# Kernel tuning notes

Hardware: AMD Instinct MI355X
Metric: run time of the kernel (lower is better)

The kernel has to match this reference:

```python
import jax, jax.numpy as jnp
import numpy as np
from jax import lax

T, B = 32, 16
NUM_ACTIONS = 18
HID = 256
C_V, C_K, C_S, NQ = 120, 8, 64, 4
NKEY, NVAL = C_K + C_S, C_V + C_S
Hh, Ww = 27, 20


def _spatial_basis():
    # Fourier spatial basis from Mott et al.; U = V = 8 -> 64 channels.
    h, w, U = Hh, Ww, 8
    p_h = np.arange(1, h + 1)[:, None] * np.ones((1, w)) * (np.pi / h)
    p_w = np.ones((h, 1)) * np.arange(1, w + 1)[None, :] * (np.pi / w)
    u = np.arange(1, U + 1)
    a = np.cos(p_h[:, :, None] * u)  # (h,w,8)
    b = np.cos(p_w[:, :, None] * u)  # (h,w,8)
    S = np.einsum('hwu,hwv->hwuv', a, b).reshape(h, w, U * U)
    return jnp.asarray(S, jnp.float32)

_S = _spatial_basis()


def _conv(x, w, b, stride, pad):
    y = lax.conv_general_dilated(x, w, stride, pad,
                                 dimension_numbers=('NCHW', 'OIHW', 'NCHW'))
    return y + b[None, :, None, None]


def setup_inputs() -> dict:
    key = jax.random.key(0)
    ks = iter(jax.random.split(key, 40))
    f32 = jnp.float32
    def rn(shape, s=0.05):
        return jax.random.normal(next(ks), shape, dtype=f32) * s
    return dict(
        frame=jax.random.normal(next(ks), (T, B, 3, 210, 160), dtype=f32),
        done=jnp.zeros((T, B), dtype=bool),
        last_action=jax.random.randint(next(ks), (T, B), 0, NUM_ACTIONS),
        reward=jax.random.normal(next(ks), (T, B), dtype=f32),
        core_h=jnp.zeros((B, HID), f32), core_c=jnp.zeros((B, HID), f32),
        conv_h=jnp.zeros((B, HID // 2, Hh, Ww), f32),
        conv_c=jnp.zeros((B, HID // 2, Hh, Ww), f32),
        cnn_w1=rn((32, 3, 8, 8)), cnn_b1=rn((32,)),
        cnn_w2=rn((64, 32, 4, 4)), cnn_b2=rn((64,)),
        lstm_w=rn((512, 192, 3, 3)), lstm_b=rn((512,)),
        qw1=rn((HID, 128)), qb1=rn((128,)),
        qw2=rn((128, NQ * NKEY)), qb2=rn((NQ * NKEY,)),
        qw3=rn((NQ * NKEY, NQ * NKEY)), qb3=rn((NQ * NKEY,)),
        aw1=rn((NVAL * NQ + NKEY * NQ + 1 + NUM_ACTIONS, 2 * HID)), ab1=rn((2 * HID,)),
        aw2=rn((2 * HID, HID)), ab2=rn((HID,)),
        w_ih=rn((4 * HID, HID)), w_hh=rn((4 * HID, HID)),
        b_ih=rn((4 * HID,)), b_hh=rn((4 * HID,)),
        pw=rn((HID, NUM_ACTIONS)), pb=rn((NUM_ACTIONS,)),
        vw=rn((HID, 1)), vb=rn((1,)),
    )


def reference(frame, done, last_action, reward, core_h, core_c, conv_h, conv_c,
              cnn_w1, cnn_b1, cnn_w2, cnn_b2, lstm_w, lstm_b,
              qw1, qb1, qw2, qb2, qw3, qb3, aw1, ab1, aw2, ab2,
              w_ih, w_hh, b_ih, b_hh, pw, pb, vw, vb):
    x = frame.reshape(T * B, 3, 210, 160)
    x = _conv(x, cnn_w1, cnn_b1, (4, 4), [(1, 1), (2, 2)])
    x = _conv(x, cnn_w2, cnn_b2, (2, 2), [(2, 2), (1, 1)])  # (T*B,64,27,20)
    x = x.reshape(T, B, 64, Hh, Ww)
    nd = (~done).astype(jnp.float32)  # (T,B)

    def vis_step(carry, inp):
        h, c = carry
        x_t, nd_t = inp
        m = nd_t[:, None, None, None]
        h, c = m * h, m * c
        gates = _conv(jnp.concatenate([x_t, h], axis=1), lstm_w, lstm_b,
                      (1, 1), [(1, 1), (1, 1)])
        ai, af, ao, ag = jnp.split(gates, 4, axis=1)
        c = jax.nn.sigmoid(af) * c + jax.nn.sigmoid(ai) * jnp.tanh(ag)
        h = jax.nn.sigmoid(ao) * jnp.tanh(c)
        return (h, c), h

    (vh, vc), O = lax.scan(vis_step, (conv_h, conv_c), (x, nd))
    # Faithful to the original `.view(N, h, w, c)` (a reinterpret, not a transpose).
    O = O.reshape(T * B, Hh, Ww, 128)
    Sb = jnp.broadcast_to(_S, (T * B, Hh, Ww, C_S))
    K = jnp.concatenate([O[..., :C_K], Sb], axis=3).reshape(T, B, Hh, Ww, NKEY)
    V = jnp.concatenate([O[..., C_K:], Sb], axis=3).reshape(T, B, Hh, Ww, NVAL)

    a1h = jax.nn.one_hot(last_action, NUM_ACTIONS, dtype=jnp.float32)  # (T,B,A)
    r = jnp.clip(reward, -1.0, 1.0)[..., None]  # (T,B,1)

    def core_step(carry, inp):
        h, c = carry
        K_t, V_t, r_t, a_t, nd_t = inp
        q = jax.nn.relu(h @ qw1 + qb1)
        q = jax.nn.relu(q @ qw2 + qb2)
        q = (q @ qw3 + qb3).reshape(B, NQ, NKEY)
        A = jnp.einsum('bhwk,bqk->bhwq', K_t, q)
        A = jax.nn.softmax(A.reshape(B, Hh * Ww, NQ), axis=1).reshape(B, Hh, Ww, NQ)
        ans = jnp.einsum('bhwq,bhwv->bqv', A, V_t)  # (B,NQ,NVAL)
        answer = jnp.concatenate(
            [ans.reshape(B, -1), q.reshape(B, -1), r_t, a_t], axis=1)
        ci = jax.nn.relu(answer @ aw1 + ab1) @ aw2 + ab2
        m = nd_t[:, None]
        h, c = m * h, m * c
        gates = ci @ w_ih.T + b_ih + h @ w_hh.T + b_hh  # torch gate order i,f,g,o
        gi, gf, gg, go = jnp.split(gates, 4, axis=1)
        c = jax.nn.sigmoid(gf) * c + jax.nn.sigmoid(gi) * jnp.tanh(gg)
        h = jax.nn.sigmoid(go) * jnp.tanh(c)
        return (h, c), h

    (ch, cc), outs = lax.scan(core_step, (core_h, core_c), (K, V, r, a1h, nd))
    out = outs.reshape(T * B, HID)
    logits = out @ pw + pb
    values = out @ vw + vb
    action = jnp.argmax(logits, axis=1)  # eval-mode action selection
    return (logits.reshape(T, B, NUM_ACTIONS), values.reshape(T, B),
            action.reshape(T, B), ch, cc, vh, vc)
```

## Files before the change

kernel.cpp:

```cpp
#include <hip/hip_runtime.h>
#include <math.h>

#define T_ 32
#define B_ 16
#define NA 18
#define P_ 540

typedef __attribute__((ext_vector_type(8)))  short short8;
typedef __attribute__((ext_vector_type(16))) float f32x16;

__device__ __forceinline__ float sigm(float x){ return 1.0f/(1.0f+expf(-x)); }
__device__ __forceinline__ unsigned short f2bf(float f){
    unsigned u = __float_as_uint(f);
    u += 0x7fff + ((u>>16)&1u);
    return (unsigned short)(u>>16);
}
__device__ __forceinline__ float bfu(unsigned short u){ return __uint_as_float(((unsigned)u)<<16); }

__global__ __launch_bounds__(256) void conv1k(const float* __restrict__ frame,
                                              const float* __restrict__ w,
                                              const float* __restrict__ bias,
                                              unsigned short* __restrict__ c1pad){
    __shared__ float tile[4032];
    int bid = blockIdx.x;
    int n = bid / 52, oh = bid % 52;
    int tid = threadIdx.x;
    const float* fb = frame + (size_t)n*3*210*160;
    for (int s = tid; s < 4032; s += 256){
        int col = s % 168;
        int row = (s/168) & 7;
        int ic  = s / 1344;
        int iy = oh*4 - 1 + row;
        int ix = col - 2;
        float v = 0.f;
        if (iy >= 0 && iy < 210 && ix >= 0 && ix < 160) v = fb[ic*33600 + iy*160 + ix];
        tile[s] = v;
    }
    __syncthreads();
    int oc = tid & 31, grp = tid >> 5;
    float acc[5] = {0.f,0.f,0.f,0.f,0.f};
    const float* wb = w + oc*192;
    for (int ic=0; ic<3; ++ic){
        #pragma unroll
        for (int kh=0; kh<8; ++kh){
            const float* wr = wb + ic*64 + kh*8;
            float4 w0 = *((const float4*)wr);
            float4 w1 = *((const float4*)(wr+4));
            const float* row = tile + ic*1344 + kh*168 + grp*20;
            float r[24];
            *((float4*)(r+ 0)) = *((const float4*)(row+ 0));
            *((float4*)(r+ 4)) = *((const float4*)(row+ 4));
            *((float4*)(r+ 8)) = *((const float4*)(row+ 8));
            *((float4*)(r+12)) = *((const float4*)(row+12));
            *((float4*)(r+16)) = *((const float4*)(row+16));
            *((float4*)(r+20)) = *((const float4*)(row+20));
            #pragma unroll
            for (int o=0;o<5;++o){
                acc[o] += r[o*4+0]*w0.x + r[o*4+1]*w0.y + r[o*4+2]*w0.z + r[o*4+3]*w0.w
                        + r[o*4+4]*w1.x + r[o*4+5]*w1.y + r[o*4+6]*w1.z + r[o*4+7]*w1.w;
            }
        }
    }
    float bi = bias[oc];
    unsigned short* ob = c1pad + ((size_t)(n*32 + oc)*56 + oh+2)*42 + 1;
    #pragma unroll
    for (int o=0;o<5;++o) ob[grp*5+o] = f2bf(acc[o] + bi);
}

__global__ void apack2k(const float* __restrict__ w2, unsigned short* __restrict__ ap){
    int idx = blockIdx.x*256 + threadIdx.x;
    if (idx >= 32768) return;
    int j = idx & 7;
    int lane = (idx>>3) & 63;
    int mt = (idx>>9) & 1;
    int ic = idx >> 10;
    int k = ((lane>>5)<<3) + j;
    int oc = mt*32 + (lane & 31);
    ap[idx] = f2bf(w2[((oc*32 + ic)<<4) + k]);
}

__global__ __launch_bounds__(256) void c2mfma(const unsigned short* __restrict__ c1pad,
                                              const unsigned short* __restrict__ apack2,
                                              const float* __restrict__ bias,
                                              unsigned short* __restrict__ xpad){
    __shared__ unsigned short p2[2][3072];
    __shared__ float bsm[64];
    int bid = blockIdx.x;
    int s = bid / 5;
    int n0 = (bid % 5) * 128;
    int tid = threadIdx.x;
    int wave = tid >> 6, lane = tid & 63;
    int khalf = (lane>>5) << 3;
    if (tid < 64) bsm[tid] = bias[tid];
    const unsigned short* cb = c1pad + (size_t)s*32*2352;

    int soff[8], swaddr[8];
    #pragma unroll
    for (int q=0;q<8;++q){
        int idx = q*256 + tid;
        int n = idx & 127, k = idx >> 7;
        int p = n0 + n; if (p > 539) p = 539;
        soff[q] = ((p/20)*2 + (k>>2))*42 + (p%20)*2 + (k&3);
        swaddr[q] = n*24 + k;
    }
    #pragma unroll
    for (int q=0;q<8;++q) p2[0][swaddr[q]] = cb[soff[q]];
    unsigned short rv[8];
    #pragma unroll
    for (int q=0;q<8;++q) rv[q] = cb[2352 + soff[q]];

    int mt = wave >> 1, ntb = (wave & 1) * 2;
    short8 acur = *((const short8*)(apack2 + ((size_t)mt*64 + lane)*8));
    short8 anxt;
    f32x16 acc[2];
    #pragma unroll
    for (int jj=0;jj<2;++jj)
        #pragma unroll
        for (int rg=0;rg<16;++rg) acc[jj][rg] = 0.f;
    __syncthreads();

    for (int c=0; c<32; ++c){
        int buf = c & 1;
        if (c < 31){
            #pragma unroll
            for (int q=0;q<8;++q) p2[buf^1][swaddr[q]] = rv[q];
        }
        if (c < 30){
            const unsigned short* src = cb + (size_t)(c+2)*2352;
            #pragma unroll
            for (int q=0;q<8;++q) rv[q] = src[soff[q]];
        }
        if (c < 31) anxt = *((const short8*)(apack2 + ((size_t)((c+1)*2 + mt)*64 + lane)*8));
        #pragma unroll
        for (int jj=0;jj<2;++jj){
            int n = (ntb+jj)*32 + (lane & 31);
            short8 bf = *((const short8*)(&p2[buf][n*24 + khalf]));
            acc[jj] = __builtin_amdgcn_mfma_f32_32x32x16_bf16(acur, bf, acc[jj], 0, 0, 0);
        }
        acur = anxt;
        __syncthreads();
    }
    #pragma unroll
    for (int jj=0;jj<2;++jj){
        int pos = n0 + (ntb+jj)*32 + (lane & 31);
        if (pos >= 540) continue;
        int y = pos/20, x = pos%20;
        unsigned short* op = xpad + (size_t)s*64*640 + (y+1)*22 + x + 1;
        #pragma unroll
        for (int rg=0; rg<16; ++rg){
            int oc = mt*32 + (rg & 3) + 8*(rg>>2) + 4*(lane>>5);
            op[(size_t)oc*640] = f2bf(acc[jj][rg] + bsm[oc]);
        }
    }
}

__global__ void sbasisk(float* __restrict__ S){
    int idx = blockIdx.x*256 + threadIdx.x;
    if (idx >= P_*64) return;
    int s = idx & 63, p = idx >> 6;
    int y = p/20, x = p%20;
    int u = s >> 3, v = s & 7;
    double a  = cos((double)((y+1)*(u+1)) * M_PI / 27.0);
    double bb = cos((double)((x+1)*(v+1)) * M_PI / 20.0);
    S[idx] = (float)(a*bb);
}

__global__ void packw4k(const float* __restrict__ in, unsigned short* __restrict__ out, int R, int C){
    int idx = blockIdx.x*256 + threadIdx.x;
    int r4cnt = (R+3)>>2;
    if (idx >= r4cnt*C*4) return;
    int j = idx & 3;
    int rc = idx >> 2;
    int c = rc % C;
    int r = (rc / C)*4 + j;
    out[idx] = (r < R) ? f2bf(in[(size_t)r*C + c]) : (unsigned short)0;
}
__global__ void packt4k(const float* __restrict__ in, unsigned short* __restrict__ out, int R, int C){
    int idx = blockIdx.x*256 + threadIdx.x;
    int r4cnt = (R+3)>>2;
    if (idx >= r4cnt*C*4) return;
    int j = idx & 3;
    int rc = idx >> 2;
    int c = rc % C;
    int r = (rc / C)*4 + j;
    out[idx] = (r < R) ? f2bf(in[(size_t)c*R + r]) : (unsigned short)0;
}

__global__ void apackk(const float* __restrict__ lw, unsigned short* __restrict__ ap){
    int idx = blockIdx.x*256 + threadIdx.x;
    if (idx >= 1572864) return;
    int j = idx & 7;
    int lane = (idx>>3) & 63;
    int mt = (idx>>9) & 15;
    int ch = idx >> 13;
    int kk = ((lane>>5)<<3) + j;
    int oc = mt*32 + (lane & 31);
    ap[idx] = (kk < 9) ? f2bf(lw[(size_t)oc*1728 + ch*9 + kk]) : (unsigned short)0;
}

__global__ void h0packk(const float* __restrict__ h0, unsigned short* __restrict__ hpad){
    int idx = blockIdx.x*256 + threadIdx.x;
    if (idx >= 16*128*540) return;
    int plane = idx / 540, p = idx % 540;
    hpad[(size_t)plane*640 + (p/20+1)*22 + (p%20) + 1] = f2bf(h0[idx]);
}

__global__ __launch_bounds__(512) void gvck(const unsigned short* __restrict__ xpad,
                                            const unsigned short* __restrict__ hrd,
                                            unsigned short* __restrict__ hwr,
                                            const unsigned short* __restrict__ apack,
                                            const float* __restrict__ lb,
                                            const unsigned char* __restrict__ done,
                                            float* __restrict__ vh, float* __restrict__ vc,
                                            unsigned short* __restrict__ hreA,
                                            const float* __restrict__ S,
                                            const unsigned short* __restrict__ pq1, const float* __restrict__ qb1,
                                            const unsigned short* __restrict__ pq2, const float* __restrict__ qb2,
                                            const unsigned short* __restrict__ pq3, const float* __restrict__ qb3,
                                            const unsigned short* __restrict__ pa1, const float* __restrict__ ab1,
                                            const unsigned short* __restrict__ pa2, const float* __restrict__ ab2,
                                            const unsigned short* __restrict__ pih, const unsigned short* __restrict__ phh,
                                            const float* __restrict__ bih, const float* __restrict__ bhh,
                                            const float* __restrict__ reward, const int* __restrict__ lact,
                                            float* __restrict__ hsb, float* __restrict__ csb,
                                            float* __restrict__ outs,
                                            int t){
    __shared__ __align__(16) unsigned char smraw[65536];
    int bid = blockIdx.x;
    int tid = threadIdx.x;

    if (bid < 288){
        if (t >= T_) return;
        unsigned short (*panel)[6144] = (unsigned short (*)[6144])smraw;
        float* gsm = (float*)smraw;
        int b  = bid % 16;
        int r  = bid / 16;
        int nb = r % 9;
        int mh = r / 9;
        int wave = tid >> 6, lane = tid & 63;
        int khalf = (lane>>5) << 3;
        int n0 = nb * 64;
        bool dn = done[t*B_ + b];

        const unsigned short* xb = xpad + ((size_t)(t*B_ + b))*64*640;
        const unsigned short* hb = hrd + (size_t)b*128*640;

        int soff[5], swaddr[5], gq[5];
        bool act[5];
        #pragma unroll
        for (int q=0;q<5;++q){
            int idx = q*512 + tid;
            act[q] = idx < 2304;
            int idc = act[q] ? idx : 0;
            int g = idc / 576;
            int rr = idc % 576;
            int k = rr / 64, n = rr & 63;
            int p = n0 + n; if (p > 539) p = 539;
            int pbase = (p/20)*22 + (p%20);
            soff[q] = pbase + (k/3)*22 + (k%3);
            swaddr[q] = g*1536 + n*24 + k;
            gq[q] = g;
        }
        for (int s2 = tid; s2 < 3584; s2 += 512){
            int bf2 = s2 / 1792, r2 = s2 % 1792;
            int g2 = r2 / 448, rr2 = r2 % 448;
            panel[bf2][g2*1536 + (rr2 & 63)*24 + 9 + (rr2>>6)] = 0;
        }
        #pragma unroll
        for (int q=0;q<5;++q) if (act[q]) panel[0][swaddr[q]] = xb[gq[q]*640 + soff[q]];
        unsigned short rv[5];
        #pragma unroll
        for (int q=0;q<5;++q) rv[q] = act[q] ? xb[(4+gq[q])*640 + soff[q]] : (unsigned short)0;

        int mt = (wave>>1)*4 + mh*2 + (wave&1);
        short8 acur[4], anxt[4];
        #pragma unroll
        for (int kc=0;kc<4;++kc)
            acur[kc] = *((const short8*)(apack + ((size_t)(kc*16 + mt)*64 + lane)*8));

        f32x16 acc[2];
        #pragma unroll
        for (int j=0;j<2;++j)
            #pragma unroll
            for (int rg=0;rg<16;++rg) acc[j][rg] = 0.f;
        __syncthreads();

        for (int it=0; it<48; ++it){
            int buf = it & 1;
            if (it < 47){
                #pragma unroll
                for (int q=0;q<5;++q) if (act[q]) panel[buf^1][swaddr[q]] = rv[q];
            }
            if (it < 46){
                int icb = (it+2)*4;
                #pragma unroll
                for (int q=0;q<5;++q){
                    if (act[q]){
                        int ic = icb + gq[q];
                        rv[q] = (ic < 64) ? xb[ic*640 + soff[q]]
                                          : (dn ? (unsigned short)0 : hb[(ic-64)*640 + soff[q]]);
                    }
                }
            }
            if (it < 47){
                int cb2 = (it+1)*4;
                #pragma unroll
                for (int kc=0;kc<4;++kc)
                    anxt[kc] = *((const short8*)(apack + ((size_t)((cb2+kc)*16 + mt)*64 + lane)*8));
            }
            #pragma unroll
            for (int kc=0;kc<4;++kc){
                #pragma unroll
                for (int j=0;j<2;++j){
                    int n = j*32 + (lane & 31);
                    short8 bf = *((const short8*)(&panel[buf][kc*1536 + n*24 + khalf]));
                    acc[j] = __builtin_amdgcn_mfma_f32_32x32x16_bf16(acur[kc], bf, acc[j], 0, 0, 0);
                }
            }
            #pragma unroll
            for (int kc=0;kc<4;++kc) acur[kc] = anxt[kc];
            __syncthreads();
        }

        int g8 = wave >> 1, ih = wave & 1;
        #pragma unroll
        for (int j=0;j<2;++j){
            int p_loc = j*32 + (lane & 31);
            #pragma unroll
            for (int rg=0; rg<16; ++rg){
                int c_loc = ih*32 + 4*(lane>>5) + (rg & 3) + 8*(rg>>2);
                gsm[g8*4096 + c_loc*64 + p_loc] = acc[j][rg];
            }
        }
        __syncthreads();

        {
            int p_loc = tid & 63, c0 = tid >> 6;
            int pg = n0 + p_loc;
            if (pg < 540){
                float m = dn ? 0.f : 1.f;
                int y = pg/20, x = pg%20;
                #pragma unroll
                for (int e=0;e<8;++e){
                    int c_loc = c0*8 + e;
                    int cg = mh*64 + c_loc;
                    float gi = gsm[        c_loc*64 + p_loc] + lb[      cg];
                    float gf = gsm[ 4096 + c_loc*64 + p_loc] + lb[128 + cg];
                    float go = gsm[ 8192 + c_loc*64 + p_loc] + lb[256 + cg];
                    float gg = gsm[12288 + c_loc*64 + p_loc] + lb[384 + cg];
                    size_t idx = ((size_t)b*128 + cg)*540 + pg;
                    float cold = vc[idx] * m;
                    float cn = sigm(gf)*cold + sigm(gi)*tanhf(gg);
                    float hn = sigm(go)*tanhf(cn);
                    vc[idx] = cn;
                    if (t == T_-1) vh[idx] = hn;
                    hwr[((size_t)b*128 + cg)*640 + (y+1)*22 + x + 1] = f2bf(hn);
                    int flat = cg*540 + pg;
                    int pos = (flat/2560)*20 + (flat/128)%20;
                    int ch  = flat & 127;
                    hreA[((size_t)(t*B_ + b)*540 + pos)*128 + ch] = f2bf(hn);
                }
            }
        }
        return;
    }

    if (t == 0) return;
    int tc = t - 1;
    int b = bid - 288;
    float* fs = (float*)smraw;
    float* hs   = fs;
    float* cs   = fs + 256;
    float* hs2  = fs + 512;
    float* q1   = fs + 768;
    float* q2   = fs + 896;
    float* q3   = fs + 1184;
    float* elog = fs + 1472;
    float* red  = fs + 3632;
    float* ansv = fs + 3664;
    float* hid  = fs + 4720;
    float* cis  = fs + 5232;
    float* gb   = fs + 5488;

    if (tid < 256){ hs[tid] = hsb[b*256+tid]; cs[tid] = csb[b*256+tid]; }
    if (tid >= 256 && tid < 269) ansv[1043 + (tid-256)] = 0.f;
    __syncthreads();

    float m = done[tc*B_+b] ? 0.f : 1.f;
    if (tid < 128){
        float a0=0.f,a1=0.f,a2=0.f,a3=0.f;
        for (int i4=0;i4<64;++i4){
            ushort4 w = *((const ushort4*)(pq1 + (size_t)((i4<<7)+tid)*4));
            float4 h4 = *((const float4*)(hs + i4*4));
            a0 += h4.x*bfu(w.x); a1 += h4.y*bfu(w.y);
            a2 += h4.z*bfu(w.z); a3 += h4.w*bfu(w.w);
        }
        q1[tid] = fmaxf(qb1[tid] + ((a0+a1)+(a2+a3)), 0.f);
    }
    __syncthreads();
    if (tid < 288){
        float a0=0.f,a1=0.f,a2=0.f,a3=0.f;
        for (int i4=0;i4<32;++i4){
            ushort4 w = *((const ushort4*)(pq2 + (size_t)(i4*288+tid)*4));
            float4 h4 = *((const float4*)(q1 + i4*4));
            a0 += h4.x*bfu(w.x); a1 += h4.y*bfu(w.y);
            a2 += h4.z*bfu(w.z); a3 += h4.w*bfu(w.w);
        }
        q2[tid] = fmaxf(qb2[tid] + ((a0+a1)+(a2+a3)), 0.f);
    }
    __syncthreads();
    if (tid < 288){
        float a0=0.f,a1=0.f,a2=0.f,a3=0.f;
        for (int i4=0;i4<72;++i4){
            ushort4 w = *((const ushort4*)(pq3 + (size_t)(i4*288+tid)*4));
            float4 h4 = *((const float4*)(q2 + i4*4));
            a0 += h4.x*bfu(w.x); a1 += h4.y*bfu(w.y);
            a2 += h4.z*bfu(w.z); a3 += h4.w*bfu(w.w);
        }
        float a = qb3[tid] + ((a0+a1)+(a2+a3));
        q3[tid] = a;
        ansv[736+tid] = a;
    }
    if (tid == 0){ float r = reward[tc*B_+b]; ansv[1024] = fminf(1.f,fmaxf(-1.f,r)); }
    if (tid >= 32 && tid < 32+NA) ansv[1025 + tid-32] = (lact[tc*B_+b] == tid-32) ? 1.f : 0.f;
    __syncthreads();

    const unsigned short* hrb = hreA + (size_t)(tc*B_ + b)*540*128;
    for (int idx = tid; idx < 4*P_; idx += 512){
        int qi = idx / P_, p = idx % P_;
        const unsigned short* hp = hrb + (size_t)p*128;
        uint4 hv = *((const uint4*)hp);
        const float* qv = q3 + qi*72;
        float a = __uint_as_float(hv.x<<16)*qv[0] + __uint_as_float(hv.x & 0xffff0000u)*qv[1]
                + __uint_as_float(hv.y<<16)*qv[2] + __uint_as_float(hv.y & 0xffff0000u)*qv[3]
                + __uint_as_float(hv.z<<16)*qv[4] + __uint_as_float(hv.z & 0xffff0000u)*qv[5]
                + __uint_as_float(hv.w<<16)*qv[6] + __uint_as_float(hv.w & 0xffff0000u)*qv[7];
        const float* Sp = S + p*64;
        #pragma unroll
        for (int s2=0;s2<16;++s2){
            float4 sv = *((const float4*)(Sp + 4*s2));
            a += sv.x*qv[8+4*s2] + sv.y*qv[9+4*s2] + sv.z*qv[10+4*s2] + sv.w*qv[11+4*s2];
        }
        elog[qi*P_ + p] = a;
    }
    __syncthreads();
    {
        int qi = tid >> 7, lt = tid & 127;
        float mx = -1e30f;
        for (int p = lt; p < P_; p += 128) mx = fmaxf(mx, elog[qi*P_ + p]);
        for (int off=32; off; off>>=1) mx = fmaxf(mx, __shfl_down(mx, off));
        if ((tid & 63) == 0) red[tid>>6] = mx;
        __syncthreads();
        if (tid < 4) red[16+tid] = fmaxf(red[2*tid], red[2*tid+1]);
        __syncthreads();
        mx = red[16+qi];
        float sm = 0.f;
        for (int p = lt; p < P_; p += 128){ float e = expf(elog[qi*P_ + p]-mx); elog[qi*P_ + p] = e; sm += e; }
        for (int off=32; off; off>>=1) sm += __shfl_down(sm, off);
        if ((tid & 63) == 0) red[8 + (tid>>6)] = sm;
        __syncthreads();
        if (tid < 4) red[24+tid] = red[8+2*tid] + red[8+2*tid+1];
        __syncthreads();
    }
    if (tid < 240){
        int g = tid >> 2;
        int qi = g / 15, vb = g % 15;
        int pc = tid & 3;
        float ac[8] = {0,0,0,0,0,0,0,0};
        const unsigned short* hb8 = hrb + 8 + vb*8;
        for (int p = pc*135; p < pc*135+135; ++p){
            float e = elog[qi*P_ + p];
            uint4 hv = *((const uint4*)(hb8 + (size_t)p*128));
            ac[0] += e*__uint_as_float(hv.x<<16);
            ac[1] += e*__uint_as_float(hv.x & 0xffff0000u);
            ac[2] += e*__uint_as_float(hv.y<<16);
            ac[3] += e*__uint_as_float(hv.y & 0xffff0000u);
            ac[4] += e*__uint_as_float(hv.z<<16);
            ac[5] += e*__uint_as_float(hv.z & 0xffff0000u);
            ac[6] += e*__uint_as_float(hv.w<<16);
            ac[7] += e*__uint_as_float(hv.w & 0xffff0000u);
        }
        #pragma unroll
        for (int j=0;j<8;++j){ ac[j] += __shfl_down(ac[j],2); ac[j] += __shfl_down(ac[j],1); }
        if ((tid&3)==0){
            float inv2 = 1.f/red[24+qi];
            #pragma unroll
            for (int j=0;j<8;++j) ansv[qi*184 + vb*8 + j] = ac[j]*inv2;
        }
    } else if (tid < 496){
        int u = tid - 240;
        int g = u >> 2;
        int qi = g >> 4, vb4 = g & 15;
        int pc = u & 3;
        float ac[4] = {0,0,0,0};
        const float* Sp = S + vb4*4;
        for (int p = pc*135; p < pc*135+135; ++p){
            float e = elog[qi*P_ + p];
            float4 sv = *((const float4*)(Sp + (size_t)p*64));
            ac[0]+=e*sv.x; ac[1]+=e*sv.y; ac[2]+=e*sv.z; ac[3]+=e*sv.w;
        }
        #pragma unroll
        for (int j=0;j<4;++j){ ac[j] += __shfl_down(ac[j],2); ac[j] += __shfl_down(ac[j],1); }
        if ((tid&3)==0){
            float inv2 = 1.f/red[24+qi];
            #pragma unroll
            for (int j=0;j<4;++j) ansv[qi*184 + 120 + vb4*4 + j] = ac[j]*inv2;
        }
    }
    __syncthreads();
    {
        float a0=ab1[tid], a1=0.f, a2=0.f, a3=0.f;
        for (int i4=0;i4<261;++i4){
            ushort4 w = *((const ushort4*)(pa1 + (size_t)((i4<<9)+tid)*4));
            float4 av = *((const float4*)(ansv + i4*4));
            a0 += av.x*bfu(w.x); a1 += av.y*bfu(w.y);
            a2 += av.z*bfu(w.z); a3 += av.w*bfu(w.w);
        }
        hid[tid] = fmaxf((a0+a1)+(a2+a3), 0.f);
    }
    if (tid < 256) hs2[tid] = hs[tid]*m;
    __syncthreads();
    if (tid < 256){
        float a0=ab2[tid],a1=0.f,a2=0.f,a3=0.f;
        for (int i4=0;i4<128;++i4){
            ushort4 w = *((const ushort4*)(pa2 + (size_t)((i4<<8)+tid)*4));
            float4 hv = *((const float4*)(hid + i4*4));
            a0 += hv.x*bfu(w.x); a1 += hv.y*bfu(w.y);
            a2 += hv.z*bfu(w.z); a3 += hv.w*bfu(w.w);
        }
        cis[tid] = (a0+a1)+(a2+a3);
    }
    __syncthreads();
    for (int g = tid; g < 1024; g += 512){
        float a0=bih[g]+bhh[g], a1=0.f, a2=0.f, a3=0.f;
        for (int i4=0;i4<64;++i4){
            ushort4 wi = *((const ushort4*)(pih + (size_t)((i4<<10)+g)*4));
            ushort4 wh = *((const ushort4*)(phh + (size_t)((i4<<10)+g)*4));
            float4 cv = *((const float4*)(cis + i4*4));
            float4 hv = *((const float4*)(hs2 + i4*4));
            a0 += cv.x*bfu(wi.x) + hv.x*bfu(wh.x);
            a1 += cv.y*bfu(wi.y) + hv.y*bfu(wh.y);
            a2 += cv.z*bfu(wi.z) + hv.z*bfu(wh.z);
            a3 += cv.w*bfu(wi.w) + hv.w*bfu(wh.w);
        }
        gb[g] = (a0+a1)+(a2+a3);
    }
    __syncthreads();
    if (tid < 256){
        float gi = gb[tid], gf = gb[256+tid], gg = gb[512+tid], go = gb[768+tid];
        float cold = cs[tid]*m;
        float cn = sigm(gf)*cold + sigm(gi)*tanhf(gg);
        float hn = sigm(go)*tanhf(cn);
        csb[b*256+tid] = cn;
        hsb[b*256+tid] = hn;
        outs[(tc*B_+b)*256+tid] = hn;
    }
}

__global__ __launch_bounds__(64) void finalk(const float* __restrict__ outs,
                                             const float* __restrict__ pw, const float* __restrict__ pb,
                                             const float* __restrict__ vw, const float* __restrict__ vb,
                                             float* __restrict__ dout){
    int row = blockIdx.x, tid = threadIdx.x;
    __shared__ float os[256];
    __shared__ float lg[NA];
    for (int i=tid; i<256; i+=64) os[i] = outs[row*256+i];
    __syncthreads();
    if (tid < NA){
        float a = pb[tid];
        for (int i=0;i<256;++i) a += os[i]*pw[i*NA+tid];
        lg[tid] = a;
        dout[row*NA + tid] = a;
    } else if (tid == 32){
        float a = vb[0];
        for (int i=0;i<256;++i) a += os[i]*vw[i];
        dout[9216 + row] = a;
    }
    __syncthreads();
    if (tid == 0){
        int am = 0; float bv = lg[0];
        for (int j=1;j<NA;++j) if (lg[j] > bv){ bv = lg[j]; am = j; }
        dout[9728 + row] = (float)am;
    }
}

extern "C" void kernel_launch(void* const* d_in, const int* in_sizes, int n_in,
                              void* d_out, int out_size, void* d_ws, size_t ws_size,
                              hipStream_t stream) {
    const float* frame   = (const float*)d_in[0];
    const unsigned char* done = (const unsigned char*)d_in[1];
    const int*   lact    = (const int*)d_in[2];
    const float* reward  = (const float*)d_in[3];
    const float* core_h0 = (const float*)d_in[4];
    const float* core_c0 = (const float*)d_in[5];
    const float* conv_h0 = (const float*)d_in[6];
    const float* conv_c0 = (const float*)d_in[7];
    const float* cnn_w1  = (const float*)d_in[8];
    const float* cnn_b1  = (const float*)d_in[9];
    const float* cnn_w2  = (const float*)d_in[10];
    const float* cnn_b2  = (const float*)d_in[11];
    const float* lstm_w  = (const float*)d_in[12];
    const float* lstm_b  = (const float*)d_in[13];
    const float* qw1 = (const float*)d_in[14]; const float* qb1 = (const float*)d_in[15];
    const float* qw2 = (const float*)d_in[16]; const float* qb2 = (const float*)d_in[17];
    const float* qw3 = (const float*)d_in[18]; const float* qb3 = (const float*)d_in[19];
    const float* aw1 = (const float*)d_in[20]; const float* ab1 = (const float*)d_in[21];
    const float* aw2 = (const float*)d_in[22]; const float* ab2 = (const float*)d_in[23];
    const float* w_ih = (const float*)d_in[24]; const float* w_hh = (const float*)d_in[25];
    const float* b_ih = (const float*)d_in[26]; const float* b_hh = (const float*)d_in[27];
    const float* pw = (const float*)d_in[28]; const float* pb = (const float*)d_in[29];
    const float* vw = (const float*)d_in[30]; const float* vb = (const float*)d_in[31];

    float* ws = (float*)d_ws;
    float* dout = (float*)d_out;

    unsigned short* xpad   = (unsigned short*)ws;
    unsigned short* c1pad  = (unsigned short*)(ws + 10485760);
    unsigned short* hreA   = (unsigned short*)(ws + 10485760);
    unsigned short* apack  = (unsigned short*)(ws + 28180480);
    unsigned short* wpk    = (unsigned short*)(ws + 28966912);
    unsigned short* pq1 = wpk;
    unsigned short* pq2 = wpk + 32768;
    unsigned short* pq3 = wpk + 69632;
    unsigned short* pa1 = wpk + 152576;
    unsigned short* pa2 = wpk + 687104;
    unsigned short* pih = wpk + 818176;
    unsigned short* phh = wpk + 1080320;
    unsigned short* hpad0  = (unsigned short*)(ws + 29753344);
    unsigned short* apack2 = (unsigned short*)(ws + 30408704);
    unsigned short* hpad1  = (unsigned short*)(ws + 30425088);
    float* hsb   = ws + 31080448;
    float* csb   = ws + 31084544;
    float* vh    = ws + 34881536;
    float* vc    = ws + 35987456;
    float* S     = ws + 37093376;
    float* outs  = ws + 37127936;

    hipMemsetAsync(xpad,  0, (size_t)20971520*2, stream);
    hipMemsetAsync(c1pad, 0, (size_t)38535168*2, stream);

    apack2k<<<128, 256, 0, stream>>>(cnn_w2, apack2);
    conv1k<<<512*52, 256, 0, stream>>>(frame, cnn_w1, cnn_b1, c1pad);
    c2mfma<<<2560, 256, 0, stream>>>(c1pad, apack2, cnn_b2, xpad);

    hipMemsetAsync(hpad0, 0, (size_t)1310720*2, stream);
    hipMemsetAsync(hpad1, 0, (size_t)1310720*2, stream);
    sbasisk<<<135, 256, 0, stream>>>(S);
    apackk<<<6144, 256, 0, stream>>>(lstm_w, apack);
    packw4k<<<128,  256, 0, stream>>>(qw1, pq1, 256, 128);
    packw4k<<<144,  256, 0, stream>>>(qw2, pq2, 128, 288);
    packw4k<<<324,  256, 0, stream>>>(qw3, pq3, 288, 288);
    packw4k<<<2088, 256, 0, stream>>>(aw1, pa1, 1043, 512);
    packw4k<<<512,  256, 0, stream>>>(aw2, pa2, 512, 256);
    packt4k<<<1024, 256, 0, stream>>>(w_ih, pih, 256, 1024);
    packt4k<<<1024, 256, 0, stream>>>(w_hh, phh, 256, 1024);
    h0packk<<<4320, 256, 0, stream>>>(conv_h0, hpad0);
    hipMemcpyAsync(vc,  conv_c0, (size_t)16*128*540*sizeof(float), hipMemcpyDeviceToDevice, stream);
    hipMemcpyAsync(hsb, core_h0, (size_t)16*256*sizeof(float), hipMemcpyDeviceToDevice, stream);
    hipMemcpyAsync(csb, core_c0, (size_t)16*256*sizeof(float), hipMemcpyDeviceToDevice, stream);

    for (int t = 0; t <= T_; ++t){
        gvck<<<304, 512, 0, stream>>>(xpad, (t&1)?hpad1:hpad0, (t&1)?hpad0:hpad1,
                                      apack, lstm_b, done, vh, vc, hreA,
                                      S, pq1,qb1,pq2,qb2,pq3,qb3,
                                      pa1,ab1,pa2,ab2, pih,phh,b_ih,b_hh,
                                      reward, lact, hsb, csb, outs, t);
    }

    finalk<<<512, 64, 0, stream>>>(outs, pw, pb, vw, vb, dout);

    hipMemcpyAsync(dout + 10240,   outs + (size_t)31*B_*256, (size_t)16*256*sizeof(float), hipMemcpyDeviceToDevice, stream);
    hipMemcpyAsync(dout + 14336,   csb, (size_t)16*256*sizeof(float), hipMemcpyDeviceToDevice, stream);
    hipMemcpyAsync(dout + 18432,   vh,  (size_t)16*128*540*sizeof(float), hipMemcpyDeviceToDevice, stream);
    hipMemcpyAsync(dout + 1124352, vc,  (size_t)16*128*540*sizeof(float), hipMemcpyDeviceToDevice, stream);
}
```

Baseline: 5.549 ms.

## Restructure ConvLSTM gate conv as tap-major implicit GEMM with channel-last smem tile

The ConvLSTM gate convolution stops padding each channel's 9-tap kernel up to 16 (wasting 7/16 of the MFMA K dimension). It now loops over the 9 taps with K running over 16 channels, reading a channel-last shared-memory slab of 6 padded rows that is loaded once, which replaces the 48-step double-buffered gather pipeline. Weights are repacked tap-major to match. Separately, conv1 computes two output rows per block to reuse weight loads and halve the block count. Risks are LDS bank conflicts from the 200-short channel stride, transposed scalar stores into shared memory, and weight fetches inside the loop without prefetch.

```diff
diff --git a/kernel.cpp b/kernel.cpp
--- a/kernel.cpp
+++ b/kernel.cpp
@@ -21,15 +21,15 @@
                                               const float* __restrict__ w,
                                               const float* __restrict__ bias,
                                               unsigned short* __restrict__ c1pad){
-    __shared__ float tile[4032];
+    __shared__ float tile[6048];
     int bid = blockIdx.x;
-    int n = bid / 52, oh = bid % 52;
+    int n = bid / 26, oh = (bid % 26)*2;
     int tid = threadIdx.x;
     const float* fb = frame + (size_t)n*3*210*160;
-    for (int s = tid; s < 4032; s += 256){
+    for (int s = tid; s < 6048; s += 256){
         int col = s % 168;
-        int row = (s/168) & 7;
-        int ic  = s / 1344;
+        int row = (s/168) % 12;
+        int ic  = s / 2016;
         int iy = oh*4 - 1 + row;
         int ix = col - 2;
         float v = 0.f;
@@ -38,7 +38,7 @@
     }
     __syncthreads();
     int oc = tid & 31, grp = tid >> 5;
-    float acc[5] = {0.f,0.f,0.f,0.f,0.f};
+    float acc[10] = {0.f,0.f,0.f,0.f,0.f,0.f,0.f,0.f,0.f,0.f};
     const float* wb = w + oc*192;
     for (int ic=0; ic<3; ++ic){
         #pragma unroll
@@ -46,25 +46,40 @@
             const float* wr = wb + ic*64 + kh*8;
             float4 w0 = *((const float4*)wr);
             float4 w1 = *((const float4*)(wr+4));
-            const float* row = tile + ic*1344 + kh*168 + grp*20;
+            const float* rowA = tile + ic*2016 + kh*168 + grp*20;
             float r[24];
-            *((float4*)(r+ 0)) = *((const float4*)(row+ 0));
-            *((float4*)(r+ 4)) = *((const float4*)(row+ 4));
-            *((float4*)(r+ 8)) = *((const float4*)(row+ 8));
-            *((float4*)(r+12)) = *((const float4*)(row+12));
-            *((float4*)(r+16)) = *((const float4*)(row+16));
-            *((float4*)(r+20)) = *((const float4*)(row+20));
+            *((float4*)(r+ 0)) = *((const float4*)(rowA+ 0));
+            *((float4*)(r+ 4)) = *((const float4*)(rowA+ 4));
+            *((float4*)(r+ 8)) = *((const float4*)(rowA+ 8));
+            *((float4*)(r+12)) = *((const float4*)(rowA+12));
+            *((float4*)(r+16)) = *((const float4*)(rowA+16));
+            *((float4*)(r+20)) = *((const float4*)(rowA+20));
             #pragma unroll
             for (int o=0;o<5;++o){
                 acc[o] += r[o*4+0]*w0.x + r[o*4+1]*w0.y + r[o*4+2]*w0.z + r[o*4+3]*w0.w
                         + r[o*4+4]*w1.x + r[o*4+5]*w1.y + r[o*4+6]*w1.z + r[o*4+7]*w1.w;
             }
+            const float* rowB = rowA + 672;
+            *((float4*)(r+ 0)) = *((const float4*)(rowB+ 0));
+            *((float4*)(r+ 4)) = *((const float4*)(rowB+ 4));
+            *((float4*)(r+ 8)) = *((const float4*)(rowB+ 8));
+            *((float4*)(r+12)) = *((const float4*)(rowB+12));
+            *((float4*)(r+16)) = *((const float4*)(rowB+16));
+            *((float4*)(r+20)) = *((const float4*)(rowB+20));
+            #pragma unroll
+            for (int o=0;o<5;++o){
+                acc[5+o] += r[o*4+0]*w0.x + r[o*4+1]*w0.y + r[o*4+2]*w0.z + r[o*4+3]*w0.w
+                          + r[o*4+4]*w1.x + r[o*4+5]*w1.y + r[o*4+6]*w1.z + r[o*4+7]*w1.w;
+            }
         }
     }
     float bi = bias[oc];
     unsigned short* ob = c1pad + ((size_t)(n*32 + oc)*56 + oh+2)*42 + 1;
     #pragma unroll
     for (int o=0;o<5;++o) ob[grp*5+o] = f2bf(acc[o] + bi);
+    ob += 42;
+    #pragma unroll
+    for (int o=0;o<5;++o) ob[grp*5+o] = f2bf(acc[5+o] + bi);
 }
 
 __global__ void apack2k(const float* __restrict__ w2, unsigned short* __restrict__ ap){
@@ -186,16 +201,17 @@
     out[idx] = (r < R) ? f2bf(in[(size_t)c*R + r]) : (unsigned short)0;
 }
 
-__global__ void apackk(const float* __restrict__ lw, unsigned short* __restrict__ ap){
+__global__ void apack9k(const float* __restrict__ lw, unsigned short* __restrict__ ap){
     int idx = blockIdx.x*256 + threadIdx.x;
-    if (idx >= 1572864) return;
+    if (idx >= 884736) return;
     int j = idx & 7;
     int lane = (idx>>3) & 63;
     int mt = (idx>>9) & 15;
-    int ch = idx >> 13;
-    int kk = ((lane>>5)<<3) + j;
+    int f  = idx >> 13;
+    int tap = f / 12, c = f % 12;
+    int ch = c*16 + ((lane>>5)<<3) + j;
     int oc = mt*32 + (lane & 31);
-    ap[idx] = (kk < 9) ? f2bf(lw[(size_t)oc*1728 + ch*9 + kk]) : (unsigned short)0;
+    ap[idx] = f2bf(lw[(size_t)oc*1728 + ch*9 + tap]);
 }
 
 __global__ void h0packk(const float* __restrict__ h0, unsigned short* __restrict__ hpad){
@@ -231,7 +247,7 @@
 
     if (bid < 288){
         if (t >= T_) return;
-        unsigned short (*panel)[6144] = (unsigned short (*)[6144])smraw;
+        unsigned short* sm = (unsigned short*)smraw;
         float* gsm = (float*)smraw;
         int b  = bid % 16;
         int r  = bid / 16;
@@ -240,87 +256,59 @@
         int wave = tid >> 6, lane = tid & 63;
         int khalf = (lane>>5) << 3;
         int n0 = nb * 64;
+        int y0 = n0 / 20;
         bool dn = done[t*B_ + b];
 
         const unsigned short* xb = xpad + ((size_t)(t*B_ + b))*64*640;
         const unsigned short* hb = hrd + (size_t)b*128*640;
 
-        int soff[5], swaddr[5], gq[5];
-        bool act[5];
-        #pragma unroll
-        for (int q=0;q<5;++q){
-            int idx = q*512 + tid;
-            act[q] = idx < 2304;
-            int idc = act[q] ? idx : 0;
-            int g = idc / 576;
-            int rr = idc % 576;
-            int k = rr / 64, n = rr & 63;
-            int p = n0 + n; if (p > 539) p = 539;
-            int pbase = (p/20)*22 + (p%20);
-            soff[q] = pbase + (k/3)*22 + (k%3);
-            swaddr[q] = g*1536 + n*24 + k;
-            gq[q] = g;
-        }
-        for (int s2 = tid; s2 < 3584; s2 += 512){
-            int bf2 = s2 / 1792, r2 = s2 % 1792;
-            int g2 = r2 / 448, rr2 = r2 % 448;
-            panel[bf2][g2*1536 + (rr2 & 63)*24 + 9 + (rr2>>6)] = 0;
-        }
-        #pragma unroll
-        for (int q=0;q<5;++q) if (act[q]) panel[0][swaddr[q]] = xb[gq[q]*640 + soff[q]];
-        unsigned short rv[5];
-        #pragma unroll
-        for (int q=0;q<5;++q) rv[q] = act[q] ? xb[(4+gq[q])*640 + soff[q]] : (unsigned short)0;
+        for (int rr = tid; rr < 1152; rr += 512){
+            int ch = rr / 6, r6 = rr % 6;
+            int prow = y0 + r6;
+            unsigned short* dst = sm + (r6*22)*200 + ch;
+            if (prow <= 28 && !(dn && ch >= 64)){
+                const unsigned short* srcp = (ch < 64) ? (xb + ch*640 + prow*22)
+                                                       : (hb + (ch-64)*640 + prow*22);
+                const unsigned int* s32 = (const unsigned int*)srcp;
+                #pragma unroll
+                for (int c2=0;c2<11;++c2){
+                    unsigned int v = s32[c2];
+                    dst[(2*c2)*200]   = (unsigned short)(v & 0xffffu);
+                    dst[(2*c2+1)*200] = (unsigned short)(v >> 16);
+                }
+            } else {
+                #pragma unroll
+                for (int c2=0;c2<22;++c2) dst[c2*200] = 0;
+            }
+        }
 
         int mt = (wave>>1)*4 + mh*2 + (wave&1);
-        short8 acur[4], anxt[4];
-        #pragma unroll
-        for (int kc=0;kc<4;++kc)
-            acur[kc] = *((const short8*)(apack + ((size_t)(kc*16 + mt)*64 + lane)*8));
-
+        int sb[2];
+        #pragma unroll
+        for (int jj=0;jj<2;++jj){
+            int p = n0 + jj*32 + (lane & 31); if (p > 539) p = 539;
+            sb[jj] = ((p/20) - y0)*22 + (p%20);
+        }
         f32x16 acc[2];
         #pragma unroll
-        for (int j=0;j<2;++j)
-            #pragma unroll
-            for (int rg=0;rg<16;++rg) acc[j][rg] = 0.f;
-        __syncthreads();
-
-        for (int it=0; it<48; ++it){
-            int buf = it & 1;
-            if (it < 47){
-                #pragma unroll
-                for (int q=0;q<5;++q) if (act[q]) panel[buf^1][swaddr[q]] = rv[q];
+        for (int jj=0;jj<2;++jj)
+            #pragma unroll
+            for (int rg=0;rg<16;++rg) acc[jj][rg] = 0.f;
+        __syncthreads();
+
+        for (int tap=0; tap<9; ++tap){
+            int tadd = (tap/3)*22 + (tap%3);
+            #pragma unroll
+            for (int c=0;c<12;++c){
+                short8 af = *((const short8*)(apack + ((size_t)((tap*12+c)*16 + mt)*64 + lane)*8));
+                int ch0 = c*16 + khalf;
+                short8 b0 = *((const short8*)(&sm[(sb[0]+tadd)*200 + ch0]));
+                short8 b1 = *((const short8*)(&sm[(sb[1]+tadd)*200 + ch0]));
+                acc[0] = __builtin_amdgcn_mfma_f32_32x32x16_bf16(af, b0, acc[0], 0, 0, 0);
+                acc[1] = __builtin_amdgcn_mfma_f32_32x32x16_bf16(af, b1, acc[1], 0, 0, 0);
             }
-            if (it < 46){
-                int icb = (it+2)*4;
-                #pragma unroll
-                for (int q=0;q<5;++q){
-                    if (act[q]){
-                        int ic = icb + gq[q];
-                        rv[q] = (ic < 64) ? xb[ic*640 + soff[q]]
-                                          : (dn ? (unsigned short)0 : hb[(ic-64)*640 + soff[q]]);
-                    }
-                }
-            }
-            if (it < 47){
-                int cb2 = (it+1)*4;
-                #pragma unroll
-                for (int kc=0;kc<4;++kc)
-                    anxt[kc] = *((const short8*)(apack + ((size_t)((cb2+kc)*16 + mt)*64 + lane)*8));
-            }
-            #pragma unroll
-            for (int kc=0;kc<4;++kc){
-                #pragma unroll
-                for (int j=0;j<2;++j){
-                    int n = j*32 + (lane & 31);
-                    short8 bf = *((const short8*)(&panel[buf][kc*1536 + n*24 + khalf]));
-                    acc[j] = __builtin_amdgcn_mfma_f32_32x32x16_bf16(acur[kc], bf, acc[j], 0, 0, 0);
-                }
-            }
-            #pragma unroll
-            for (int kc=0;kc<4;++kc) acur[kc] = anxt[kc];
-            __syncthreads();
-        }
+        }
+        __syncthreads();
 
         int g8 = wave >> 1, ih = wave & 1;
         #pragma unroll
@@ -640,13 +628,13 @@
     hipMemsetAsync(c1pad, 0, (size_t)38535168*2, stream);
 
     apack2k<<<128, 256, 0, stream>>>(cnn_w2, apack2);
-    conv1k<<<512*52, 256, 0, stream>>>(frame, cnn_w1, cnn_b1, c1pad);
+    conv1k<<<512*26, 256, 0, stream>>>(frame, cnn_w1, cnn_b1, c1pad);
     c2mfma<<<2560, 256, 0, stream>>>(c1pad, apack2, cnn_b2, xpad);
 
     hipMemsetAsync(hpad0, 0, (size_t)1310720*2, stream);
     hipMemsetAsync(hpad1, 0, (size_t)1310720*2, stream);
     sbasisk<<<135, 256, 0, stream>>>(S);
-    apackk<<<6144, 256, 0, stream>>>(lstm_w, apack);
+    apack9k<<<3456, 256, 0, stream>>>(lstm_w, apack);
     packw4k<<<128,  256, 0, stream>>>(qw1, pq1, 256, 128);
     packw4k<<<144,  256, 0, stream>>>(qw2, pq2, 128, 288);
     packw4k<<<324,  256, 0, stream>>>(qw3, pq3, 288, 288);
```

Result: faster. 4.929 ms (-11.2%).
